# Kernel optimization log

Measured on AMD Instinct MI355X. Metric: run time of the kernel, lower is better.

The kernel has to match this reference:

```python
import jax, jax.numpy as jnp
import numpy as np

B, N, D, S, H = 64, 4096, 256, 8, 512
ITERS = 3
EPS = 1e-8
SCALE = D ** -0.5
LN_EPS = 1e-5


def _ln(x, w, b):
    mu = jnp.mean(x, axis=-1, keepdims=True)
    var = jnp.var(x, axis=-1, keepdims=True)
    return (x - mu) * jax.lax.rsqrt(var + LN_EPS) * w + b


def setup_inputs() -> dict:
    key = jax.random.key(0)
    ks = jax.random.split(key, 20)
    g = lambda k, shape, s=0.02: jax.random.normal(k, shape, dtype=jnp.float32) * s
    return {
        "inputs": jax.random.normal(ks[0], (B, N, D), dtype=jnp.float32),
        "query_pos": jax.random.uniform(ks[1], (1, S, D), dtype=jnp.float32),
        "wq": g(ks[2], (D, D)), "bq": jnp.zeros((D,), jnp.float32),
        "wk": g(ks[3], (D, D)), "bk": jnp.zeros((D,), jnp.float32),
        "wv": g(ks[4], (D, D)), "bv": jnp.zeros((D,), jnp.float32),
        "w_ih": g(ks[5], (3 * D, D)), "b_ih": jnp.zeros((3 * D,), jnp.float32),
        "w_hh": g(ks[6], (3 * D, D)), "b_hh": jnp.zeros((3 * D,), jnp.float32),
        "w1": g(ks[7], (H, D)), "b1": jnp.zeros((H,), jnp.float32),
        "w2": g(ks[8], (D, H)), "b2": jnp.zeros((D,), jnp.float32),
        "ln_in_w": jnp.ones((D,), jnp.float32), "ln_in_b": jnp.zeros((D,), jnp.float32),
        "ln_s_w": jnp.ones((D,), jnp.float32), "ln_s_b": jnp.zeros((D,), jnp.float32),
        "ln_ff_w": jnp.ones((D,), jnp.float32), "ln_ff_b": jnp.zeros((D,), jnp.float32),
    }


def _step(slots, k, v, wq, bq, w_ih, b_ih, w_hh, b_hh, w1, b1, w2, b2,
          ln_s_w, ln_s_b, ln_ff_w, ln_ff_b):
    s = _ln(slots, ln_s_w, ln_s_b)
    q = s @ wq.T + bq                                  # [B,S,D]
    dots = jnp.einsum('bid,bjd->bij', q, k) * SCALE    # [B,S,N]
    attn = jax.nn.softmax(dots, axis=1) + EPS          # softmax over slots
    attn = attn / jnp.sum(attn, axis=-1, keepdims=True)
    updates = jnp.einsum('bjd,bij->bid', v, attn)      # [B,S,D]
    # GRUCell(input=updates, hidden=slots), PyTorch gate order r,z,n
    gx = updates @ w_ih.T + b_ih
    gh = slots @ w_hh.T + b_hh
    xr, xz, xn = jnp.split(gx, 3, axis=-1)
    hr, hz, hn = jnp.split(gh, 3, axis=-1)
    r = jax.nn.sigmoid(xr + hr)
    z = jax.nn.sigmoid(xz + hz)
    n = jnp.tanh(xn + r * hn)
    h = (1.0 - z) * n + z * slots
    ff = jnp.maximum(_ln(h, ln_ff_w, ln_ff_b) @ w1.T + b1, 0.0) @ w2.T + b2
    return h + ff


def reference(inputs, query_pos, wq, bq, wk, bk, wv, bv,
              w_ih, b_ih, w_hh, b_hh, w1, b1, w2, b2,
              ln_in_w, ln_in_b, ln_s_w, ln_s_b, ln_ff_w, ln_ff_b):
    b = inputs.shape[0]
    slots = jnp.broadcast_to(query_pos, (b, S, D))
    x = _ln(inputs, ln_in_w, ln_in_b)
    k = x @ wk.T + bk
    v = x @ wv.T + bv
    step = lambda s: _step(s, k, v, wq, bq, w_ih, b_ih, w_hh, b_hh,
                           w1, b1, w2, b2, ln_s_w, ln_s_b, ln_ff_w, ln_ff_b)
    for _ in range(ITERS):
        slots = step(slots)
    slots = step(jax.lax.stop_gradient(slots))
    return slots
```

## Files before the change

### kernel.cpp

```cpp
#include <hip/hip_runtime.h>
#include <hip/hip_bf16.h>

#define DEV __device__ __forceinline__
typedef unsigned short u16;
using s16x8  = __attribute__((ext_vector_type(8))) short;
using f32x4v = __attribute__((ext_vector_type(4))) float;

constexpr float SCALE  = 0.0625f;
constexpr float EPS    = 1e-8f;
constexpr float LN_EPS = 1e-5f;

DEV u16 f2bf(float f) {
    __hip_bfloat16 h = __float2bfloat16(f);
    u16 u; __builtin_memcpy(&u, &h, 2); return u;
}
DEV float bf2f(u16 u) {
    unsigned int x = ((unsigned int)u) << 16;
    float f; __builtin_memcpy(&f, &x, 4); return f;
}
DEV float ld1(const void* p, size_t i, int bf) {
    return bf ? bf2f(((const u16*)p)[i]) : ((const float*)p)[i];
}
DEV float warp_sum64(float v) {
    v += __shfl_xor(v, 1);  v += __shfl_xor(v, 2);  v += __shfl_xor(v, 4);
    v += __shfl_xor(v, 8);  v += __shfl_xor(v, 16); v += __shfl_xor(v, 32);
    return v;
}
DEV float sigf(float x) { return 1.f / (1.f + expf(-x)); }

__global__ void k_sniff(const void* __restrict__ x, int* __restrict__ flag) {
    int lane = threadIdx.x;
    u16 u = ((const u16*)x)[lane * 2];
    float v = bf2f(u);
    bool bad = !(fabsf(v) <= 1024.0f);
    unsigned long long m = __ballot(bad);
    if (lane == 0) *flag = (m == 0ull) ? 1 : 0;
}

__global__ __launch_bounds__(256) void k_prep_misc(
    const void* bq, const void* bk, const void* bv, const void* bih, const void* bhh,
    const void* b1, const void* b2, const void* liw, const void* lib,
    const void* lsw, const void* lsb, const void* lfw, const void* lfb,
    float* o_bq, float* o_bk, float* o_bv, float* o_bih, float* o_bhh,
    float* o_b1, float* o_b2, float* o_liw, float* o_lib,
    float* o_lsw, float* o_lsb, float* o_lfw, float* o_lfb,
    const int* flagp) {
    int bf = *flagp;
    int i = blockIdx.x * 256 + threadIdx.x;
    if (i < 256) { o_bq[i]  = ld1(bq,  i, bf); return; } i -= 256;
    if (i < 256) { o_bk[i]  = ld1(bk,  i, bf); return; } i -= 256;
    if (i < 256) { o_bv[i]  = ld1(bv,  i, bf); return; } i -= 256;
    if (i < 768) { o_bih[i] = ld1(bih, i, bf); return; } i -= 768;
    if (i < 768) { o_bhh[i] = ld1(bhh, i, bf); return; } i -= 768;
    if (i < 512) { o_b1[i]  = ld1(b1,  i, bf); return; } i -= 512;
    if (i < 256) { o_b2[i]  = ld1(b2,  i, bf); return; } i -= 256;
    if (i < 256) { o_liw[i] = ld1(liw, i, bf); return; } i -= 256;
    if (i < 256) { o_lib[i] = ld1(lib, i, bf); return; } i -= 256;
    if (i < 256) { o_lsw[i] = ld1(lsw, i, bf); return; } i -= 256;
    if (i < 256) { o_lsb[i] = ld1(lsb, i, bf); return; } i -= 256;
    if (i < 256) { o_lfw[i] = ld1(lfw, i, bf); return; } i -= 256;
    if (i < 256) { o_lfb[i] = ld1(lfb, i, bf); }
}

__global__ __launch_bounds__(256) void k_prep_w(
    const void* wq, const void* wv, const void* wk,
    const void* wih, const void* whh, const void* w1, const void* w2,
    u16* wqT_b, u16* wvT_b, u16* wk2_b, u16* wih_b, u16* whh_b, u16* w1_b, u16* w2_b,
    const float* __restrict__ liw, const int* flagp) {
    int bf = *flagp;
    int i = blockIdx.x * 256 + threadIdx.x;
    if (i < 65536)  { int c=i>>8, d=i&255; wqT_b[i] = f2bf(ld1(wq, (size_t)d*256+c, bf)); return; } i -= 65536;
    if (i < 65536)  { int c=i>>8, d=i&255; wvT_b[i] = f2bf(ld1(wv, (size_t)d*256+c, bf)); return; } i -= 65536;
    if (i < 65536)  { int n=i>>8, d=i&255; wk2_b[i] = f2bf(ld1(wk, (size_t)d*256+n, bf) * liw[n]); return; } i -= 65536;
    if (i < 196608) { wih_b[i] = f2bf(ld1(wih, i, bf)); return; } i -= 196608;
    if (i < 196608) { whh_b[i] = f2bf(ld1(whh, i, bf)); return; } i -= 196608;
    if (i < 131072) { w1_b[i]  = f2bf(ld1(w1,  i, bf)); return; } i -= 131072;
    if (i < 131072) { w2_b[i]  = f2bf(ld1(w2,  i, bf)); }
}

__global__ __launch_bounds__(256) void k_prep_m(const void* __restrict__ wk,
    const float* __restrict__ liw, const float* __restrict__ lib,
    const float* __restrict__ bk_f, float* __restrict__ m1p, float* __restrict__ m2p,
    const int* flagp) {
    int bf = *flagp;
    int wave = threadIdx.x >> 6, lane = threadIdx.x & 63;
    int d = blockIdx.x * 4 + wave;
    float s1 = 0.f, s2 = 0.f;
#pragma unroll
    for (int t = 0; t < 4; t++) {
        int c = lane * 4 + t;
        float w = ld1(wk, (size_t)d * 256 + c, bf);
        s1 += w * lib[c];
        s2 += w * liw[c];
    }
    s1 = warp_sum64(s1); s2 = warp_sum64(s2);
    if (lane == 0) { m1p[d] = s1 + bk_f[d]; m2p[d] = -s2; }
}

__global__ __launch_bounds__(256) void k_prep_u(
    const void* __restrict__ wq, const void* __restrict__ wk, const void* __restrict__ wih,
    const float* __restrict__ m1p, const float* __restrict__ m2p,
    const float* __restrict__ bq_f, const float* __restrict__ bv_f,
    const float* __restrict__ liw,
    float* __restrict__ u1, float* __restrict__ u2, float* __restrict__ bq2,
    float* __restrict__ wibv, float* __restrict__ c12, const int* flagp) {
    int bf = *flagp;
    int wave = threadIdx.x >> 6, lane = threadIdx.x & 63;
    int idx = blockIdx.x * 4 + wave;
    if (idx >= 1538) return;
    float s = 0.f;
#pragma unroll
    for (int t = 0; t < 4; t++) {
        int d = lane * 4 + t;
        if (idx < 256)       s += ld1(wq, (size_t)d*256 + idx, bf) * m1p[d];
        else if (idx < 512)  s += ld1(wq, (size_t)d*256 + (idx-256), bf) * m2p[d];
        else if (idx < 768)  s += bq_f[d] * ld1(wk, (size_t)d*256 + (idx-512), bf);
        else if (idx < 1536) s += ld1(wih, (size_t)(idx-768)*256 + d, bf) * bv_f[d];
        else if (idx == 1536) s += bq_f[d] * m1p[d];
        else                  s += bq_f[d] * m2p[d];
    }
    s = warp_sum64(s);
    if (lane == 0) {
        if (idx < 256)       u1[idx] = s;
        else if (idx < 512)  u2[idx-256] = s;
        else if (idx < 768)  bq2[idx-512] = s * liw[idx-512];
        else if (idx < 1536) wibv[idx-768] = s;
        else                 c12[idx-1536] = s;
    }
}

__global__ __launch_bounds__(256) void k_conv(const void* __restrict__ x,
    u16* __restrict__ XB, u16* __restrict__ XT,
    float* __restrict__ mu, float* __restrict__ rs, const int* flagp) {
    int bf = *flagp;
    int jt = blockIdx.x;
    int b  = blockIdx.y;
    int tid = threadIdx.x;
    int j = tid >> 2, q = tid & 3;
    size_t rowg = (size_t)b * 4096 + jt * 64 + j;
    __shared__ u16 LT[256 * 72];
    float s = 0.f, s2 = 0.f;
#pragma unroll
    for (int cc = 0; cc < 16; ++cc) {
        int c0 = cc * 16 + q * 4;
        float v[4];
        if (bf) {
            u16 a4[4];
            __builtin_memcpy(a4, (const u16*)x + rowg * 256 + c0, 8);
#pragma unroll
            for (int e = 0; e < 4; e++) v[e] = bf2f(a4[e]);
        } else {
            float4 f = *(const float4*)((const float*)x + rowg * 256 + c0);
            v[0] = f.x; v[1] = f.y; v[2] = f.z; v[3] = f.w;
        }
        u16 b4[4];
#pragma unroll
        for (int e = 0; e < 4; e++) {
            s += v[e]; s2 += v[e] * v[e];
            b4[e] = f2bf(v[e]);
            LT[(c0 + e) * 72 + j] = b4[e];
        }
        __builtin_memcpy(XB + rowg * 256 + c0, b4, 8);
    }
    s  += __shfl_xor(s, 1);   s  += __shfl_xor(s, 2);
    s2 += __shfl_xor(s2, 1);  s2 += __shfl_xor(s2, 2);
    if (q == 0) {
        float m = s * (1.f / 256.f);
        mu[rowg] = m;
        rs[rowg] = rsqrtf(s2 * (1.f / 256.f) - m * m + LN_EPS);
    }
    __syncthreads();
    int c = tid;
    s16x8 seg[8];
#pragma unroll
    for (int k = 0; k < 8; ++k)
        seg[k] = *(const s16x8*)(LT + c * 72 + k * 8);
    u16* dst = XT + ((size_t)b * 256 + c) * 4096 + jt * 64;
#pragma unroll
    for (int k = 0; k < 8; ++k)
        *(s16x8*)(dst + k * 8) = seg[k];
}

__global__ __launch_bounds__(256) void k_prep_s(const void* __restrict__ qp,
    const float* __restrict__ lsw, const float* __restrict__ lsb,
    const float* __restrict__ u1, const float* __restrict__ u2, const float* __restrict__ c12,
    float* __restrict__ slots, u16* __restrict__ Acat, u16* __restrict__ s_b,
    float* __restrict__ kap, float* __restrict__ lam, const int* flagp) {
    int bf = *flagp;
    int m = blockIdx.x;
    int s_ = m & 7, d = threadIdx.x;
    float v = ld1(qp, (size_t)s_ * 256 + d, bf);
    slots[(size_t)m*256 + d]   = v;
    Acat[(size_t)m*512 + 256 + d] = f2bf(v);
    __shared__ float red[16];
    float su = warp_sum64(v), sq = warp_sum64(v*v);
    int wave = threadIdx.x >> 6, lane = threadIdx.x & 63;
    if (lane == 0) { red[wave] = su; red[4+wave] = sq; }
    __syncthreads();
    float S1 = red[0]+red[1]+red[2]+red[3], S2 = red[4]+red[5]+red[6]+red[7];
    float muv = S1*(1.f/256.f);
    float rsv = rsqrtf(S2*(1.f/256.f) - muv*muv + LN_EPS);
    float sn = (v - muv)*rsv*lsw[d] + lsb[d];
    s_b[(size_t)m*256 + d] = f2bf(sn);
    float ks = warp_sum64(sn * u1[d]), ls = warp_sum64(sn * u2[d]);
    if (lane == 0) { red[8+wave] = ks; red[12+wave] = ls; }
    __syncthreads();
    if (threadIdx.x == 0) {
        kap[m] = red[8]+red[9]+red[10]+red[11] + c12[0];
        lam[m] = red[12]+red[13]+red[14]+red[15] + c12[1];
    }
}

template<bool OUT_BF16, bool RELU>
__global__ __launch_bounds__(256) void gemm64(
    const u16* __restrict__ A, const u16* __restrict__ W,
    const float* __restrict__ bias, void* __restrict__ outp, int Nn, int K) {
    int m0 = blockIdx.x * 64, n0 = blockIdx.y * 64;
    int tid = threadIdx.x;
    int wave = tid >> 6, lane = tid & 63, quad = lane >> 4, l15 = lane & 15;
    int wm = wave >> 1, wn = wave & 1;
    __shared__ __attribute__((aligned(16))) u16 A_s[64*40];
    __shared__ __attribute__((aligned(16))) u16 B_s[64*40];
    f32x4v acc[2][2];
#pragma unroll
    for (int i = 0; i < 2; i++)
#pragma unroll
        for (int j = 0; j < 2; j++) acc[i][j] = (f32x4v){0.f,0.f,0.f,0.f};
    int r0 = tid >> 2, seg = tid & 3;
    int nkc = K >> 5;
    for (int kc = 0; kc < nkc; ++kc) {
        s16x8 a0 = *(const s16x8*)(A + (size_t)(m0 + r0)*K + kc*32 + seg*8);
        s16x8 b0 = *(const s16x8*)(W + (size_t)(n0 + r0)*K + kc*32 + seg*8);
        __syncthreads();
        *(s16x8*)(A_s + r0*40 + seg*8) = a0;
        *(s16x8*)(B_s + r0*40 + seg*8) = b0;
        __syncthreads();
        s16x8 af[2], bfr[2];
#pragma unroll
        for (int t = 0; t < 2; t++) af[t]  = *(const s16x8*)(A_s + (wm*32 + t*16 + l15)*40 + quad*8);
#pragma unroll
        for (int t = 0; t < 2; t++) bfr[t] = *(const s16x8*)(B_s + (wn*32 + t*16 + l15)*40 + quad*8);
#pragma unroll
        for (int ti = 0; ti < 2; ti++)
#pragma unroll
            for (int tj = 0; tj < 2; tj++)
                acc[ti][tj] = __builtin_amdgcn_mfma_f32_16x16x32_bf16(af[ti], bfr[tj], acc[ti][tj], 0, 0, 0);
    }
#pragma unroll
    for (int tj = 0; tj < 2; tj++) {
        int colg = n0 + wn*32 + tj*16 + l15;
        float bv_ = bias ? bias[colg] : 0.f;
#pragma unroll
        for (int ti = 0; ti < 2; ti++) {
            int rowb = m0 + wm*32 + ti*16 + quad*4;
#pragma unroll
            for (int r = 0; r < 4; r++) {
                float v = acc[ti][tj][r] + bv_;
                if (RELU) v = fmaxf(v, 0.f);
                if (OUT_BF16) ((u16*)outp)[(size_t)(rowb + r)*Nn + colg] = f2bf(v);
                else          ((float*)outp)[(size_t)(rowb + r)*Nn + colg] = v;
            }
        }
    }
}

__global__ __launch_bounds__(256) void k_big(const u16* __restrict__ Wc2_b,
    const u16* __restrict__ whh_b, const float* __restrict__ bih_f,
    const float* __restrict__ bhh_f, const float* __restrict__ wibv,
    u16* __restrict__ Wbig, float* __restrict__ bbig) {
    int idx = blockIdx.x * 256 + threadIdx.x;
    int n = idx >> 9, k = idx & 511;
    u16 v;
    if (n < 512)      v = (k < 256) ? Wc2_b[(size_t)n*256 + k] : whh_b[(size_t)n*256 + (k-256)];
    else if (n < 768) v = (k < 256) ? Wc2_b[(size_t)n*256 + k] : (u16)0;
    else              v = (k < 256) ? (u16)0 : whh_b[(size_t)(n-256)*256 + (k-256)];
    Wbig[idx] = v;
    if (idx < 1024) {
        float bb;
        if (idx < 512)      bb = bih_f[idx] + wibv[idx] + bhh_f[idx];
        else if (idx < 768) bb = bih_f[idx] + wibv[idx];
        else                bb = bhh_f[idx-256];
        bbig[idx] = bb;
    }
}

__global__ __launch_bounds__(256) void k_attn(
    const u16* __restrict__ XB, const u16* __restrict__ XT,
    const u16* __restrict__ q2b,
    const float* __restrict__ kap, const float* __restrict__ lam,
    const float* __restrict__ mu, const float* __restrict__ rs,
    float* __restrict__ Zp, float* __restrict__ Rp, float* __restrict__ Tp) {
    int jcc = blockIdx.x;
    int b   = blockIdx.y;
    int tid = threadIdx.x;
    int wave = tid >> 6, lane = tid & 63, quad = lane >> 4, l15 = lane & 15;
    __shared__ __attribute__((aligned(16))) u16 q_s[16*264];
    __shared__ __attribute__((aligned(16))) u16 a_s[16*72];
    __shared__ float kl_s[32];
    {
        int row = tid >> 5, seg = tid & 31;
        s16x8 qv = *(const s16x8*)(q2b + (size_t)(b*8 + row)*256 + seg*8);
        *(s16x8*)(q_s + row*264 + seg*8) = qv;
        s16x8 z = {0,0,0,0,0,0,0,0};
        *(s16x8*)(q_s + (8+row)*264 + seg*8) = z;
    }
    if (tid < 16) {
        kl_s[tid]      = (tid < 8) ? kap[b*8 + tid] : 0.f;
        kl_s[16 + tid] = (tid < 8) ? lam[b*8 + tid] : 0.f;
    }
    __syncthreads();

    f32x4v accz[4];
#pragma unroll
    for (int t = 0; t < 4; t++) accz[t] = (f32x4v){0.f,0.f,0.f,0.f};
    float rtot[4] = {0.f,0.f,0.f,0.f}, ttot[4] = {0.f,0.f,0.f,0.f};
    int jb16 = wave * 16;
    const u16* xtb = XT + (size_t)b * 256 * 4096;

    for (int sub = 0; sub < 2; ++sub) {
        int jloc = (jcc*2 + sub) * 64;
        size_t rowg = (size_t)b*4096 + jloc + jb16 + l15;
        const u16* xbp = XB + rowg*256 + quad*8;
        s16x8 xv[8];
#pragma unroll
        for (int kc = 0; kc < 8; ++kc) xv[kc] = *(const s16x8*)(xbp + kc*32);
        f32x4v accd = (f32x4v){0.f,0.f,0.f,0.f};
#pragma unroll
        for (int kc = 0; kc < 8; ++kc) {
            s16x8 af = *(const s16x8*)(q_s + l15*264 + kc*32 + quad*8);
            accd = __builtin_amdgcn_mfma_f32_16x16x32_bf16(af, xv[kc], accd, 0, 0, 0);
        }
        float rsj = rs[rowg], mrj = mu[rowg] * rsj;
        float dv[4];
#pragma unroll
        for (int r = 0; r < 4; r++)
            dv[r] = SCALE*(rsj*accd[r] + mrj*kl_s[16 + quad*4 + r] + kl_s[quad*4 + r]);
        float mx = fmaxf(fmaxf(dv[0], dv[1]), fmaxf(dv[2], dv[3]));
        mx = fmaxf(mx, __shfl_xor(mx, 16));
        float ev[4];
        float sum = 0.f;
#pragma unroll
        for (int r = 0; r < 4; r++) { ev[r] = expf(dv[r] - mx); sum += ev[r]; }
        sum += __shfl_xor(sum, 16);
        float inv = 1.f / sum;
        float av[4];
#pragma unroll
        for (int r = 0; r < 4; r++) {
            float a = ev[r]*inv + EPS;
            rtot[r] += a;
            ttot[r] += a * mrj;
            av[r] = a * rsj;
        }
        s16x8 zv[8];
#pragma unroll
        for (int ct = 0; ct < 4; ++ct) {
            int c = wave*64 + ct*16 + l15;
#pragma unroll
            for (int kc2 = 0; kc2 < 2; ++kc2)
                zv[ct*2 + kc2] = *(const s16x8*)(xtb + (size_t)c*4096 + jloc + kc2*32 + quad*8);
        }
        __syncthreads();
#pragma unroll
        for (int r = 0; r < 4; r++)
            a_s[(quad*4 + r)*72 + jb16 + l15] = f2bf(av[r]);
        __syncthreads();
#pragma unroll
        for (int ct = 0; ct < 4; ++ct) {
#pragma unroll
            for (int kc2 = 0; kc2 < 2; ++kc2) {
                s16x8 af2 = *(const s16x8*)(a_s + l15*72 + kc2*32 + quad*8);
                accz[ct] = __builtin_amdgcn_mfma_f32_16x16x32_bf16(af2, zv[ct*2 + kc2], accz[ct], 0, 0, 0);
            }
        }
    }
    if (quad < 2) {
#pragma unroll
        for (int ct = 0; ct < 4; ++ct) {
            int c = wave*64 + ct*16 + l15;
#pragma unroll
            for (int r = 0; r < 4; r++)
                Zp[((size_t)(b*32 + jcc)*8 + quad*4 + r)*256 + c] = accz[ct][r];
        }
    }
#pragma unroll
    for (int r = 0; r < 4; r++) {
        rtot[r] += __shfl_xor(rtot[r], 1);
        rtot[r] += __shfl_xor(rtot[r], 2);
        rtot[r] += __shfl_xor(rtot[r], 4);
        rtot[r] += __shfl_xor(rtot[r], 8);
        ttot[r] += __shfl_xor(ttot[r], 1);
        ttot[r] += __shfl_xor(ttot[r], 2);
        ttot[r] += __shfl_xor(ttot[r], 4);
        ttot[r] += __shfl_xor(ttot[r], 8);
    }
    if (l15 == 0 && quad < 2) {
        int base = ((b*32 + jcc)*4 + wave)*8 + quad*4;
#pragma unroll
        for (int r = 0; r < 4; r++) { Rp[base + r] = rtot[r]; Tp[base + r] = ttot[r]; }
    }
}

__global__ __launch_bounds__(256) void k_reduce(const float* __restrict__ Zp,
    const float* __restrict__ Rp, const float* __restrict__ Tp,
    const float* __restrict__ liw, const float* __restrict__ lib,
    u16* __restrict__ Acat) {
    int m = blockIdx.x;
    int b = m >> 3, i = m & 7, d = threadIdx.x;
    float z = 0.f;
#pragma unroll
    for (int c = 0; c < 32; c++) z += Zp[((size_t)(b*32 + c)*8 + i)*256 + d];
    float rv = 0.f, tv = 0.f;
    if (d < 128) {
        rv = Rp[(size_t)(b*128 + d)*8 + i];
        tv = Tp[(size_t)(b*128 + d)*8 + i];
    }
    __shared__ float redR[4], redT[4];
    rv = warp_sum64(rv); tv = warp_sum64(tv);
    int wave = d >> 6, lane = d & 63;
    if (lane == 0) { redR[wave] = rv; redT[wave] = tv; }
    __syncthreads();
    float R = redR[0]+redR[1]+redR[2]+redR[3];
    float T = redT[0]+redT[1]+redT[2]+redT[3];
    float ys = (liw[d]*(z - T) + lib[d]*R) / R;
    Acat[(size_t)m*512 + d] = f2bf(ys);
}

__global__ __launch_bounds__(256) void k_gates(const float* __restrict__ g,
    const float* __restrict__ slots, const float* __restrict__ lfw,
    const float* __restrict__ lfb, float* __restrict__ h, u16* __restrict__ hln_b) {
    int m = blockIdx.x, d = threadIdx.x;
    const float* gm = g + (size_t)m*1024;
    float r = sigf(gm[d]);
    float z = sigf(gm[256 + d]);
    float nn = tanhf(gm[512 + d] + r * gm[768 + d]);
    float hv = (1.f - z)*nn + z*slots[(size_t)m*256 + d];
    h[(size_t)m*256 + d] = hv;
    __shared__ float red[8];
    float su = warp_sum64(hv), sq = warp_sum64(hv*hv);
    int wave = threadIdx.x >> 6, lane = threadIdx.x & 63;
    if (lane == 0) { red[wave] = su; red[4+wave] = sq; }
    __syncthreads();
    float S1 = red[0]+red[1]+red[2]+red[3], S2 = red[4]+red[5]+red[6]+red[7];
    float muv = S1*(1.f/256.f);
    float rsv = rsqrtf(S2*(1.f/256.f) - muv*muv + LN_EPS);
    hln_b[(size_t)m*256 + d] = f2bf((hv - muv)*rsv*lfw[d] + lfb[d]);
}

__global__ __launch_bounds__(256) void k_residual(const float* __restrict__ h,
    const float* __restrict__ ff2, const float* __restrict__ lsw,
    const float* __restrict__ lsb, const float* __restrict__ u1,
    const float* __restrict__ u2, const float* __restrict__ c12,
    float* __restrict__ slots, u16* __restrict__ Acat, u16* __restrict__ s_b,
    float* __restrict__ kap, float* __restrict__ lam) {
    int m = blockIdx.x, d = threadIdx.x;
    float sv = h[(size_t)m*256 + d] + ff2[(size_t)m*256 + d];
    slots[(size_t)m*256 + d] = sv;
    Acat[(size_t)m*512 + 256 + d] = f2bf(sv);
    __shared__ float red[16];
    float su = warp_sum64(sv), sq = warp_sum64(sv*sv);
    int wave = threadIdx.x >> 6, lane = threadIdx.x & 63;
    if (lane == 0) { red[wave] = su; red[4+wave] = sq; }
    __syncthreads();
    float S1 = red[0]+red[1]+red[2]+red[3], S2 = red[4]+red[5]+red[6]+red[7];
    float muv = S1*(1.f/256.f);
    float rsv = rsqrtf(S2*(1.f/256.f) - muv*muv + LN_EPS);
    float sn = (sv - muv)*rsv*lsw[d] + lsb[d];
    s_b[(size_t)m*256 + d] = f2bf(sn);
    float ks = warp_sum64(sn * u1[d]), ls = warp_sum64(sn * u2[d]);
    if (lane == 0) { red[8+wave] = ks; red[12+wave] = ls; }
    __syncthreads();
    if (threadIdx.x == 0) {
        kap[m] = red[8]+red[9]+red[10]+red[11] + c12[0];
        lam[m] = red[12]+red[13]+red[14]+red[15] + c12[1];
    }
}

__global__ __launch_bounds__(256) void k_out(const float* __restrict__ slots,
                                             void* __restrict__ out, const int* flagp) {
    int bf = *flagp;
    int i = blockIdx.x * 256 + threadIdx.x;
    if (bf) ((u16*)out)[i] = f2bf(slots[i]);
    else    ((float*)out)[i] = slots[i];
}

extern "C" void kernel_launch(void* const* d_in, const int* in_sizes, int n_in,
                              void* d_out, int out_size, void* d_ws, size_t ws_size,
                              hipStream_t stream) {
    (void)in_sizes; (void)n_in; (void)out_size; (void)ws_size;
    const void* inputs    = d_in[0];
    const void* query_pos = d_in[1];
    const void* wq   = d_in[2];  const void* bq   = d_in[3];
    const void* wk   = d_in[4];  const void* bk   = d_in[5];
    const void* wv   = d_in[6];  const void* bv   = d_in[7];
    const void* w_ih = d_in[8];  const void* b_ih = d_in[9];
    const void* w_hh = d_in[10]; const void* b_hh = d_in[11];
    const void* w1   = d_in[12]; const void* b1   = d_in[13];
    const void* w2   = d_in[14]; const void* b2   = d_in[15];
    const void* ln_in_w = d_in[16]; const void* ln_in_b = d_in[17];
    const void* ln_s_w  = d_in[18]; const void* ln_s_b  = d_in[19];
    const void* ln_ff_w = d_in[20]; const void* ln_ff_b = d_in[21];

    char* w = (char*)d_ws;
    size_t off = 0;
    auto alloc = [&](size_t bytes) -> void* {
        void* p = w + off;
        off = (off + bytes + 255) & ~(size_t)255;
        return p;
    };
    u16*   XB     = (u16*)alloc(134217728);
    u16*   XT     = (u16*)alloc(134217728);
    float* Zp     = (float*)alloc(16777216);
    float* gates  = (float*)alloc(2097152);
    u16*   Wbig_b = (u16*)alloc(1048576);
    u16*   Wc2_b  = (u16*)alloc(393216);
    u16*   Wc_b   = (u16*)alloc(131072);
    u16*   wqT_b  = (u16*)alloc(131072);
    u16*   wvT_b  = (u16*)alloc(131072);
    u16*   wk2_b  = (u16*)alloc(131072);
    u16*   wih_b  = (u16*)alloc(393216);
    u16*   whh_b  = (u16*)alloc(393216);
    u16*   w1_b   = (u16*)alloc(262144);
    u16*   w2_b   = (u16*)alloc(262144);
    float* mu     = (float*)alloc(1048576);
    float* rs     = (float*)alloc(1048576);
    float* slots  = (float*)alloc(524288);
    u16*   s_b    = (u16*)alloc(262144);
    u16*   Acat   = (u16*)alloc(524288);
    u16*   q2_b   = (u16*)alloc(262144);
    float* h      = (float*)alloc(524288);
    u16*   hln_b  = (u16*)alloc(262144);
    u16*   ff1_b  = (u16*)alloc(524288);
    float* ff2    = (float*)alloc(524288);
    float* Rp     = (float*)alloc(262144);
    float* Tp     = (float*)alloc(262144);
    float* bq_f   = (float*)alloc(1024);
    float* bk_f   = (float*)alloc(1024);
    float* bv_f   = (float*)alloc(1024);
    float* bih_f  = (float*)alloc(3072);
    float* bhh_f  = (float*)alloc(3072);
    float* b1_f   = (float*)alloc(2048);
    float* b2_f   = (float*)alloc(1024);
    float* liw_f  = (float*)alloc(1024);
    float* lib_f  = (float*)alloc(1024);
    float* lsw_f  = (float*)alloc(1024);
    float* lsb_f  = (float*)alloc(1024);
    float* lfw_f  = (float*)alloc(1024);
    float* lfb_f  = (float*)alloc(1024);
    float* m1p    = (float*)alloc(1024);
    float* m2p    = (float*)alloc(1024);
    float* u1     = (float*)alloc(1024);
    float* u2     = (float*)alloc(1024);
    float* bq2    = (float*)alloc(1024);
    float* wibv   = (float*)alloc(3072);
    float* bbig   = (float*)alloc(4096);
    float* c12    = (float*)alloc(256);
    float* kap    = (float*)alloc(2048);
    float* lam    = (float*)alloc(2048);
    int*   flag   = (int*)alloc(256);

    k_sniff<<<1, 64, 0, stream>>>(inputs, flag);
    k_prep_misc<<<18, 256, 0, stream>>>(bq, bk, bv, b_ih, b_hh, b1, b2,
                                        ln_in_w, ln_in_b, ln_s_w, ln_s_b, ln_ff_w, ln_ff_b,
                                        bq_f, bk_f, bv_f, bih_f, bhh_f, b1_f, b2_f,
                                        liw_f, lib_f, lsw_f, lsb_f, lfw_f, lfb_f, flag);
    k_conv<<<dim3(64, 64), 256, 0, stream>>>(inputs, XB, XT, mu, rs, flag);
    k_prep_w<<<3328, 256, 0, stream>>>(wq, wv, wk, w_ih, w_hh, w1, w2,
                                       wqT_b, wvT_b, wk2_b, wih_b, whh_b, w1_b, w2_b,
                                       liw_f, flag);
    k_prep_m<<<64, 256, 0, stream>>>(wk, liw_f, lib_f, bk_f, m1p, m2p, flag);
    k_prep_u<<<385, 256, 0, stream>>>(wq, wk, w_ih, m1p, m2p, bq_f, bv_f, liw_f,
                                      u1, u2, bq2, wibv, c12, flag);
    k_prep_s<<<512, 256, 0, stream>>>(query_pos, lsw_f, lsb_f, u1, u2, c12,
                                      slots, Acat, s_b, kap, lam, flag);
    gemm64<true, false><<<dim3(4, 4), 256, 0, stream>>>(wk2_b, wqT_b, nullptr, Wc_b, 256, 256);
    gemm64<true, false><<<dim3(12, 4), 256, 0, stream>>>(wih_b, wvT_b, nullptr, Wc2_b, 256, 256);
    k_big<<<2048, 256, 0, stream>>>(Wc2_b, whh_b, bih_f, bhh_f, wibv, Wbig_b, bbig);

    for (int step = 0; step < 4; ++step) {
        gemm64<true, false><<<dim3(8, 4), 256, 0, stream>>>(s_b, Wc_b, bq2, q2_b, 256, 256);
        k_attn<<<dim3(32, 64), 256, 0, stream>>>(XB, XT, q2_b, kap, lam, mu, rs, Zp, Rp, Tp);
        k_reduce<<<512, 256, 0, stream>>>(Zp, Rp, Tp, liw_f, lib_f, Acat);
        gemm64<false, false><<<dim3(8, 16), 256, 0, stream>>>(Acat, Wbig_b, bbig, gates, 1024, 512);
        k_gates<<<512, 256, 0, stream>>>(gates, slots, lfw_f, lfb_f, h, hln_b);
        gemm64<true, true ><<<dim3(8, 8), 256, 0, stream>>>(hln_b, w1_b, b1_f, ff1_b, 512, 256);
        gemm64<false, false><<<dim3(8, 4), 256, 0, stream>>>(ff1_b, w2_b, b2_f, ff2, 256, 512);
        k_residual<<<512, 256, 0, stream>>>(h, ff2, lsw_f, lsb_f, u1, u2, c12,
                                            slots, Acat, s_b, kap, lam);
    }
    k_out<<<512, 256, 0, stream>>>(slots, d_out, flag);
}
```

Before: 899.4 us.

## Vectorize conversion transpose, skip bf16 copy for bf16 inputs, double-buffer attention LDS

The conversion kernel now has each thread load 8 contiguous elements per row and reduce LayerNorm stats across 32 lanes. It stages rows in LDS and transposes on the way out. When the input is already bf16, the XB copy is no longer written and the attention kernel reads the raw input directly. The attention kernel issues the XT loads earlier so they overlap the score softmax, and double-buffers the attention-weight LDS tile so one barrier per sub-iteration can be dropped. The transpose read in LDS is now a strided gather of 16-bit elements, which may cause bank conflicts.

```diff
diff --git a/kernel.cpp b/kernel.cpp
--- a/kernel.cpp
+++ b/kernel.cpp
@@ -136,49 +136,52 @@
     int jt = blockIdx.x;
     int b  = blockIdx.y;
     int tid = threadIdx.x;
-    int j = tid >> 2, q = tid & 3;
-    size_t rowg = (size_t)b * 4096 + jt * 64 + j;
-    __shared__ u16 LT[256 * 72];
-    float s = 0.f, s2 = 0.f;
-#pragma unroll
-    for (int cc = 0; cc < 16; ++cc) {
-        int c0 = cc * 16 + q * 4;
-        float v[4];
+    __shared__ __attribute__((aligned(16))) u16 LT[64 * 264];
+    int jr   = tid >> 5;
+    int cseg = tid & 31;
+#pragma unroll
+    for (int it = 0; it < 8; ++it) {
+        int j = it * 8 + jr;
+        size_t rowg = (size_t)b * 4096 + (size_t)jt * 64 + j;
+        s16x8 val;
+        float v[8];
         if (bf) {
-            u16 a4[4];
-            __builtin_memcpy(a4, (const u16*)x + rowg * 256 + c0, 8);
-#pragma unroll
-            for (int e = 0; e < 4; e++) v[e] = bf2f(a4[e]);
+            val = *(const s16x8*)((const u16*)x + rowg * 256 + cseg * 8);
+#pragma unroll
+            for (int e = 0; e < 8; e++) v[e] = bf2f((u16)val[e]);
         } else {
-            float4 f = *(const float4*)((const float*)x + rowg * 256 + c0);
-            v[0] = f.x; v[1] = f.y; v[2] = f.z; v[3] = f.w;
-        }
-        u16 b4[4];
-#pragma unroll
-        for (int e = 0; e < 4; e++) {
-            s += v[e]; s2 += v[e] * v[e];
-            b4[e] = f2bf(v[e]);
-            LT[(c0 + e) * 72 + j] = b4[e];
-        }
-        __builtin_memcpy(XB + rowg * 256 + c0, b4, 8);
-    }
-    s  += __shfl_xor(s, 1);   s  += __shfl_xor(s, 2);
-    s2 += __shfl_xor(s2, 1);  s2 += __shfl_xor(s2, 2);
-    if (q == 0) {
-        float m = s * (1.f / 256.f);
-        mu[rowg] = m;
-        rs[rowg] = rsqrtf(s2 * (1.f / 256.f) - m * m + LN_EPS);
+            const float4* sf = (const float4*)((const float*)x + rowg * 256 + cseg * 8);
+            float4 f0 = sf[0], f1 = sf[1];
+            v[0]=f0.x; v[1]=f0.y; v[2]=f0.z; v[3]=f0.w;
+            v[4]=f1.x; v[5]=f1.y; v[6]=f1.z; v[7]=f1.w;
+#pragma unroll
+            for (int e = 0; e < 8; e++) val[e] = (short)f2bf(v[e]);
+            *(s16x8*)(XB + rowg * 256 + cseg * 8) = val;
+        }
+        *(s16x8*)(LT + j * 264 + cseg * 8) = val;
+        float ps = 0.f, ps2 = 0.f;
+#pragma unroll
+        for (int e = 0; e < 8; e++) { ps += v[e]; ps2 += v[e] * v[e]; }
+        ps  += __shfl_xor(ps, 1);  ps  += __shfl_xor(ps, 2);  ps  += __shfl_xor(ps, 4);
+        ps  += __shfl_xor(ps, 8);  ps  += __shfl_xor(ps, 16);
+        ps2 += __shfl_xor(ps2, 1); ps2 += __shfl_xor(ps2, 2); ps2 += __shfl_xor(ps2, 4);
+        ps2 += __shfl_xor(ps2, 8); ps2 += __shfl_xor(ps2, 16);
+        if (cseg == 0) {
+            float m = ps * (1.f / 256.f);
+            mu[rowg] = m;
+            rs[rowg] = rsqrtf(ps2 * (1.f / 256.f) - m * m + LN_EPS);
+        }
     }
     __syncthreads();
     int c = tid;
-    s16x8 seg[8];
-#pragma unroll
-    for (int k = 0; k < 8; ++k)
-        seg[k] = *(const s16x8*)(LT + c * 72 + k * 8);
-    u16* dst = XT + ((size_t)b * 256 + c) * 4096 + jt * 64;
-#pragma unroll
-    for (int k = 0; k < 8; ++k)
-        *(s16x8*)(dst + k * 8) = seg[k];
+    u16* dst = XT + ((size_t)b * 256 + c) * 4096 + (size_t)jt * 64;
+#pragma unroll
+    for (int k = 0; k < 8; ++k) {
+        s16x8 o;
+#pragma unroll
+        for (int t = 0; t < 8; t++) o[t] = (short)LT[(k * 8 + t) * 264 + c];
+        *(s16x8*)(dst + k * 8) = o;
+    }
 }
 
 __global__ __launch_bounds__(256) void k_prep_s(const void* __restrict__ qp,
@@ -285,17 +288,20 @@
 }
 
 __global__ __launch_bounds__(256) void k_attn(
-    const u16* __restrict__ XB, const u16* __restrict__ XT,
-    const u16* __restrict__ q2b,
+    const void* __restrict__ xraw, const u16* __restrict__ XB,
+    const u16* __restrict__ XT, const u16* __restrict__ q2b,
     const float* __restrict__ kap, const float* __restrict__ lam,
     const float* __restrict__ mu, const float* __restrict__ rs,
+    const int* __restrict__ flagp,
     float* __restrict__ Zp, float* __restrict__ Rp, float* __restrict__ Tp) {
+    int bf = *flagp;
+    const u16* xb = bf ? (const u16*)xraw : XB;
     int jcc = blockIdx.x;
     int b   = blockIdx.y;
     int tid = threadIdx.x;
     int wave = tid >> 6, lane = tid & 63, quad = lane >> 4, l15 = lane & 15;
     __shared__ __attribute__((aligned(16))) u16 q_s[16*264];
-    __shared__ __attribute__((aligned(16))) u16 a_s[16*72];
+    __shared__ __attribute__((aligned(16))) u16 a_s[2][16*72];
     __shared__ float kl_s[32];
     {
         int row = tid >> 5, seg = tid & 31;
@@ -320,7 +326,7 @@
     for (int sub = 0; sub < 2; ++sub) {
         int jloc = (jcc*2 + sub) * 64;
         size_t rowg = (size_t)b*4096 + jloc + jb16 + l15;
-        const u16* xbp = XB + rowg*256 + quad*8;
+        const u16* xbp = xb + rowg*256 + quad*8;
         s16x8 xv[8];
 #pragma unroll
         for (int kc = 0; kc < 8; ++kc) xv[kc] = *(const s16x8*)(xbp + kc*32);
@@ -329,6 +335,14 @@
         for (int kc = 0; kc < 8; ++kc) {
             s16x8 af = *(const s16x8*)(q_s + l15*264 + kc*32 + quad*8);
             accd = __builtin_amdgcn_mfma_f32_16x16x32_bf16(af, xv[kc], accd, 0, 0, 0);
+        }
+        s16x8 zv[8];
+#pragma unroll
+        for (int ct = 0; ct < 4; ++ct) {
+            int c = wave*64 + ct*16 + l15;
+#pragma unroll
+            for (int kc2 = 0; kc2 < 2; ++kc2)
+                zv[ct*2 + kc2] = *(const s16x8*)(xtb + (size_t)c*4096 + jloc + kc2*32 + quad*8);
         }
         float rsj = rs[rowg], mrj = mu[rowg] * rsj;
         float dv[4];
@@ -343,32 +357,19 @@
         for (int r = 0; r < 4; r++) { ev[r] = expf(dv[r] - mx); sum += ev[r]; }
         sum += __shfl_xor(sum, 16);
         float inv = 1.f / sum;
-        float av[4];
 #pragma unroll
         for (int r = 0; r < 4; r++) {
             float a = ev[r]*inv + EPS;
             rtot[r] += a;
             ttot[r] += a * mrj;
-            av[r] = a * rsj;
-        }
-        s16x8 zv[8];
+            a_s[sub][(quad*4 + r)*72 + jb16 + l15] = f2bf(a * rsj);
+        }
+        __syncthreads();
 #pragma unroll
         for (int ct = 0; ct < 4; ++ct) {
-            int c = wave*64 + ct*16 + l15;
-#pragma unroll
-            for (int kc2 = 0; kc2 < 2; ++kc2)
-                zv[ct*2 + kc2] = *(const s16x8*)(xtb + (size_t)c*4096 + jloc + kc2*32 + quad*8);
-        }
-        __syncthreads();
-#pragma unroll
-        for (int r = 0; r < 4; r++)
-            a_s[(quad*4 + r)*72 + jb16 + l15] = f2bf(av[r]);
-        __syncthreads();
-#pragma unroll
-        for (int ct = 0; ct < 4; ++ct) {
 #pragma unroll
             for (int kc2 = 0; kc2 < 2; ++kc2) {
-                s16x8 af2 = *(const s16x8*)(a_s + l15*72 + kc2*32 + quad*8);
+                s16x8 af2 = *(const s16x8*)(a_s[sub] + l15*72 + kc2*32 + quad*8);
                 accz[ct] = __builtin_amdgcn_mfma_f32_16x16x32_bf16(af2, zv[ct*2 + kc2], accz[ct], 0, 0, 0);
             }
         }
@@ -578,7 +579,7 @@
 
     for (int step = 0; step < 4; ++step) {
         gemm64<true, false><<<dim3(8, 4), 256, 0, stream>>>(s_b, Wc_b, bq2, q2_b, 256, 256);
-        k_attn<<<dim3(32, 64), 256, 0, stream>>>(XB, XT, q2_b, kap, lam, mu, rs, Zp, Rp, Tp);
+        k_attn<<<dim3(32, 64), 256, 0, stream>>>(inputs, XB, XT, q2_b, kap, lam, mu, rs, flag, Zp, Rp, Tp);
         k_reduce<<<512, 256, 0, stream>>>(Zp, Rp, Tp, liw_f, lib_f, Acat);
         gemm64<false, false><<<dim3(8, 16), 256, 0, stream>>>(Acat, Wbig_b, bbig, gates, 1024, 512);
         k_gates<<<512, 256, 0, stream>>>(gates, slots, lfw_f, lfb_f, h, hln_b);
```

Result: faster. 859.9 us (-4.4%).
